# Optimization experiments

Measured on AMD Instinct MI355X. Metric: run time of the kernel, lower is better.

Reference implementation:

```python
import jax, jax.numpy as jnp
import numpy as np

B = 32768
N_TABLES = 26
N_ROWS = 200000
D = 64
N_DENSE = 13
NUM_PAIRS = (N_TABLES + 1) * N_TABLES // 2  # 351, pairs j < i over 27 vectors


def setup_inputs() -> dict:
    key = jax.random.key(0)
    ks = jax.random.split(key, 16)
    def lin(kw, kb, m, n):
        W = jax.random.normal(kw, (m, n), jnp.float32) * np.sqrt(2.0 / (m + n))
        b = jax.random.normal(kb, (m,), jnp.float32) * np.sqrt(1.0 / m)
        return W, b
    bw0, bb0 = lin(ks[0], ks[1], 512, N_DENSE)
    bw1, bb1 = lin(ks[2], ks[3], 256, 512)
    bw2, bb2 = lin(ks[4], ks[5], D, 256)
    tw0, tb0 = lin(ks[6], ks[7], 512, D + NUM_PAIRS)
    tw1, tb1 = lin(ks[8], ks[9], 256, 512)
    tw2, tb2 = lin(ks[10], ks[11], 1, 256)
    bound = np.sqrt(1.0 / N_ROWS)
    emb_tables = jax.random.uniform(ks[12], (N_TABLES, N_ROWS, D), jnp.float32,
                                    minval=-bound, maxval=bound)
    dense_x = jax.random.uniform(ks[13], (B, N_DENSE), jnp.float32)
    indices = jax.random.randint(ks[14], (N_TABLES, B), 0, N_ROWS, jnp.int64)
    return {"dense_x": dense_x, "indices": indices, "emb_tables": emb_tables,
            "bw0": bw0, "bb0": bb0, "bw1": bw1, "bb1": bb1, "bw2": bw2, "bb2": bb2,
            "tw0": tw0, "tb0": tb0, "tw1": tw1, "tb1": tb1, "tw2": tw2, "tb2": tb2}


def reference(dense_x, indices, emb_tables,
              bw0, bb0, bw1, bb1, bw2, bb2,
              tw0, tb0, tw1, tb1, tw2, tb2):
    # bottom MLP (all ReLU, sigmoid_bot = -1)
    h = jax.nn.relu(dense_x @ bw0.T + bb0)
    h = jax.nn.relu(h @ bw1.T + bb1)
    x_bot = jax.nn.relu(h @ bw2.T + bb2)          # [B, D]

    # multi-table EmbeddingBag(sum) with single-index bags -> plain gather
    embs = jax.vmap(lambda tbl, idx: tbl[idx])(emb_tables, indices)  # [26, B, D]

    # dot interaction over 27 feature vectors
    T = jnp.concatenate([x_bot[None], embs], axis=0).transpose(1, 0, 2)  # [B, 27, D]
    Z = jnp.einsum('bnd,bmd->bnm', T, T)                                 # [B, 27, 27]
    li, lj = jnp.tril_indices(N_TABLES + 1, k=-1)  # pairs with j < i (no self)
    Zflat = Z[:, li, lj]                           # [B, 351]
    R = jnp.concatenate([x_bot, Zflat], axis=1)    # [B, 415]

    # top MLP: ReLU, ReLU, Sigmoid (sigmoid_top = 2)
    h = jax.nn.relu(R @ tw0.T + tb0)
    h = jax.nn.relu(h @ tw1.T + tb1)
    p = jax.nn.sigmoid(h @ tw2.T + tb2)            # [B, 1]
    return p
```

## Files before the change

### kernel.cpp

```cpp
#include <hip/hip_runtime.h>
#include <cstddef>
#include <cstdint>

#define B_SZ    32768
#define NTAB    26
#define NROWS   200000

typedef __attribute__((ext_vector_type(8))) short short8v;
typedef __attribute__((ext_vector_type(4))) float f32x4;
typedef __attribute__((ext_vector_type(16))) float f32x16;

__device__ __forceinline__ ushort f2bf(float f) {
    uint32_t u = __builtin_bit_cast(uint32_t, f);
    u += 0x7FFFu + ((u >> 16) & 1u);
    return (ushort)(u >> 16);
}
__device__ __forceinline__ float bf2f(ushort h) {
    uint32_t u = ((uint32_t)h) << 16;
    return __builtin_bit_cast(float, u);
}
__device__ __forceinline__ void stage16(const ushort* g, ushort* l) {
    __builtin_amdgcn_global_load_lds(
        (const __attribute__((address_space(1))) unsigned int*)g,
        (__attribute__((address_space(3))) unsigned int*)l, 16, 0, 0);
}

__global__ __launch_bounds__(256) void conv_all_k(
    const float* __restrict__ dense_x, const float* __restrict__ bw0,
    const float* __restrict__ tw0, const float* __restrict__ bw1,
    const float* __restrict__ bw2, const float* __restrict__ tw1,
    ushort* __restrict__ dense_pad, ushort* __restrict__ bw0p,
    ushort* __restrict__ tw0p, ushort* __restrict__ bw1c,
    ushort* __restrict__ bw2c, ushort* __restrict__ tw1c)
{
    const int gid = blockIdx.x * 256 + threadIdx.x;
    if (gid < 1048576) {
        int r = gid >> 5, k = gid & 31;
        dense_pad[gid] = (k < 13) ? f2bf(dense_x[r * 13 + k]) : (ushort)0;
    } else if (gid < 1064960) {
        int i = gid - 1048576; int r = i >> 5, k = i & 31;
        bw0p[i] = (k < 13) ? f2bf(bw0[r * 13 + k]) : (ushort)0;
    } else if (gid < 1277952) {
        int i = gid - 1064960; int r = i / 416, k = i - r * 416;
        tw0p[i] = (k < 415) ? f2bf(tw0[r * 415 + k]) : (ushort)0;
    } else if (gid < 1409024) {
        int i = gid - 1277952; bw1c[i] = f2bf(bw1[i]);
    } else if (gid < 1425408) {
        int i = gid - 1409024; bw2c[i] = f2bf(bw2[i]);
    } else if (gid < 1556480) {
        int i = gid - 1425408; tw1c[i] = f2bf(tw1[i]);
    }
}

__global__ __launch_bounds__(256, 2) void bot012_k(
    const ushort* __restrict__ dense_pad, const ushort* __restrict__ bw0p,
    const float* __restrict__ bb0, const ushort* __restrict__ bw1c,
    const float* __restrict__ bb1, const ushort* __restrict__ bw2c,
    const float* __restrict__ bb2, ushort* __restrict__ Rb)
{
    __shared__ __align__(16) ushort h0s[32 * 512];
    __shared__ __align__(16) ushort Wst[256 * 32];
    __shared__ __align__(16) ushort h1s[32 * 256];
    const int t = threadIdx.x;
    const int lane = t & 63, w = t >> 6;
    const int fr = lane & 15, j16 = lane >> 4;
    const int bBase = blockIdx.x * 32;

    if (t < 128) {
        const int r = t >> 2, u = t & 3, us = u ^ ((r >> 1) & 3);
        stage16(dense_pad + (size_t)(bBase + r) * 32 + us * 8, &h1s[t * 8]);
    }

    f32x4 acc0[2][2][4] = {};
#pragma unroll
    for (int hh = 0; hh < 2; ++hh) {
#pragma unroll
        for (int i = 0; i < 4; ++i) {
            const int idx = i * 256 + t;
            const int r = idx >> 2, u = idx & 3, us = u ^ ((r >> 1) & 3);
            stage16(bw0p + (size_t)(hh * 256 + r) * 32 + us * 8, &Wst[idx * 8]);
        }
        __syncthreads();
        short8v a[2], b[4];
#pragma unroll
        for (int m = 0; m < 2; ++m) {
            const int r = m * 16 + fr;
            a[m] = *(const short8v*)&h1s[r * 32 + (j16 ^ ((r >> 1) & 3)) * 8];
        }
#pragma unroll
        for (int n = 0; n < 4; ++n) {
            const int lr = w * 64 + n * 16 + fr;
            b[n] = *(const short8v*)&Wst[lr * 32 + (j16 ^ ((lr >> 1) & 3)) * 8];
        }
        __builtin_amdgcn_s_setprio(1);
#pragma unroll
        for (int m = 0; m < 2; ++m)
#pragma unroll
            for (int n = 0; n < 4; ++n)
                acc0[hh][m][n] = __builtin_amdgcn_mfma_f32_16x16x32_bf16(b[n], a[m], acc0[hh][m][n], 0, 0, 0);
        __builtin_amdgcn_s_setprio(0);
        __syncthreads();
    }
#pragma unroll
    for (int hh = 0; hh < 2; ++hh)
#pragma unroll
    for (int n = 0; n < 4; ++n) {
        const int ch = hh * 256 + w * 64 + n * 16 + j16 * 4;
        const float4 bv = *(const float4*)&bb0[ch];
#pragma unroll
        for (int m = 0; m < 2; ++m) {
            const int s = m * 16 + fr;
            ushort4 o;
            o.x = f2bf(fmaxf(acc0[hh][m][n][0] + bv.x, 0.f));
            o.y = f2bf(fmaxf(acc0[hh][m][n][1] + bv.y, 0.f));
            o.z = f2bf(fmaxf(acc0[hh][m][n][2] + bv.z, 0.f));
            o.w = f2bf(fmaxf(acc0[hh][m][n][3] + bv.w, 0.f));
            const int u = ch >> 3, su = u ^ (s & 7);
            *(ushort4*)&h0s[s * 512 + su * 8 + (ch & 7)] = o;
        }
    }
    __syncthreads();

    f32x4 acc1[2][4] = {};
    for (int kt = 0; kt < 512; kt += 32) {
#pragma unroll
        for (int i = 0; i < 4; ++i) {
            const int idx = i * 256 + t;
            const int r = idx >> 2, u = idx & 3, us = u ^ ((r >> 1) & 3);
            stage16(bw1c + (size_t)r * 512 + kt + us * 8, &Wst[idx * 8]);
        }
        __syncthreads();
        short8v a[2], b[4];
#pragma unroll
        for (int m = 0; m < 2; ++m) {
            const int s = m * 16 + fr;
            const int u = (kt >> 3) + j16, su = u ^ (s & 7);
            a[m] = *(const short8v*)&h0s[s * 512 + su * 8];
        }
#pragma unroll
        for (int n = 0; n < 4; ++n) {
            const int lr = w * 64 + n * 16 + fr;
            b[n] = *(const short8v*)&Wst[lr * 32 + (j16 ^ ((lr >> 1) & 3)) * 8];
        }
        __builtin_amdgcn_s_setprio(1);
#pragma unroll
        for (int m = 0; m < 2; ++m)
#pragma unroll
            for (int n = 0; n < 4; ++n)
                acc1[m][n] = __builtin_amdgcn_mfma_f32_16x16x32_bf16(b[n], a[m], acc1[m][n], 0, 0, 0);
        __builtin_amdgcn_s_setprio(0);
        __syncthreads();
    }
#pragma unroll
    for (int n = 0; n < 4; ++n) {
        const int ch = w * 64 + n * 16 + j16 * 4;
        const float4 bv = *(const float4*)&bb1[ch];
#pragma unroll
        for (int m = 0; m < 2; ++m) {
            const int s = m * 16 + fr;
            ushort4 o;
            o.x = f2bf(fmaxf(acc1[m][n][0] + bv.x, 0.f));
            o.y = f2bf(fmaxf(acc1[m][n][1] + bv.y, 0.f));
            o.z = f2bf(fmaxf(acc1[m][n][2] + bv.z, 0.f));
            o.w = f2bf(fmaxf(acc1[m][n][3] + bv.w, 0.f));
            const int u = ch >> 3, su = u ^ (s & 7);
            *(ushort4*)&h1s[s * 256 + su * 8 + (ch & 7)] = o;
        }
    }
    __syncthreads();

    f32x4 acc2[2] = {};
    for (int kt = 0; kt < 256; kt += 32) {
        {
            const int r = t >> 2, u = t & 3, us = u ^ ((r >> 1) & 3);
            stage16(bw2c + (size_t)r * 256 + kt + us * 8, &Wst[t * 8]);
        }
        __syncthreads();
        short8v a[2], b;
#pragma unroll
        for (int m = 0; m < 2; ++m) {
            const int s = m * 16 + fr;
            const int u = (kt >> 3) + j16, su = u ^ (s & 7);
            a[m] = *(const short8v*)&h1s[s * 256 + su * 8];
        }
        {
            const int lr = w * 16 + fr;
            b = *(const short8v*)&Wst[lr * 32 + (j16 ^ ((lr >> 1) & 3)) * 8];
        }
#pragma unroll
        for (int m = 0; m < 2; ++m)
            acc2[m] = __builtin_amdgcn_mfma_f32_16x16x32_bf16(b, a[m], acc2[m], 0, 0, 0);
        __syncthreads();
    }
    {
        const int ch = w * 16 + j16 * 4;
        const float4 bv = *(const float4*)&bb2[ch];
#pragma unroll
        for (int m = 0; m < 2; ++m) {
            const int s = m * 16 + fr;
            ushort4 o;
            o.x = f2bf(fmaxf(acc2[m][0] + bv.x, 0.f));
            o.y = f2bf(fmaxf(acc2[m][1] + bv.y, 0.f));
            o.z = f2bf(fmaxf(acc2[m][2] + bv.z, 0.f));
            o.w = f2bf(fmaxf(acc2[m][3] + bv.w, 0.f));
            *(ushort4*)&Rb[(size_t)(bBase + s) * 64 + ch] = o;
        }
    }
}

__global__ __launch_bounds__(256, 3) void topint_k(
    const float* __restrict__ emb, const int* __restrict__ indices,
    const ushort* __restrict__ Rb, const ushort* __restrict__ tw0p,
    const float* __restrict__ tb0, const ushort* __restrict__ tw1c,
    const float* __restrict__ tb1, const float* __restrict__ tw2,
    const float* __restrict__ tb2, float* __restrict__ out)
{
    __shared__ __align__(16) ushort U[32 * 512];
    __shared__ __align__(16) ushort Wst[256 * 32];
    __shared__ __align__(16) int scratch[832];
    const int t = threadIdx.x;
    const int lane = t & 63, w = t >> 6;
    const int fr = lane & 15, j16 = lane >> 4;
    const int bBase = blockIdx.x * 32;

    {
        const int r = t >> 3, u = t & 7;
        short8v v = *(const short8v*)&Rb[(size_t)(bBase + r) * 64 + u * 8];
        *(short8v*)&U[r * 424 + u * 8] = v;
    }
    if (t < 32) U[t * 424 + 415] = 0;
    for (int e = t; e < 832; e += 256)
        scratch[e] = indices[(size_t)(e >> 5) * B_SZ + bBase + (e & 31)];
    __syncthreads();

    {
        const int r32 = lane & 31, half = lane >> 5;
        for (int it = 0; it < 8; ++it) {
            const int s = it * 4 + w;
            short8v tf[4];
            if (r32 == 0) {
#pragma unroll
                for (int kq = 0; kq < 4; ++kq)
                    tf[kq] = *(const short8v*)&U[s * 424 + kq * 16 + half * 8];
            } else if (r32 <= 26) {
                const int idxv = scratch[(r32 - 1) * 32 + s];
                const float* rp = emb + ((size_t)(r32 - 1) * NROWS + (size_t)idxv) * 64 + half * 8;
#pragma unroll
                for (int kq = 0; kq < 4; ++kq) {
                    const float4 x = *(const float4*)&rp[kq * 16];
                    const float4 y = *(const float4*)&rp[kq * 16 + 4];
                    short8v v;
                    v[0] = (short)f2bf(x.x); v[1] = (short)f2bf(x.y);
                    v[2] = (short)f2bf(x.z); v[3] = (short)f2bf(x.w);
                    v[4] = (short)f2bf(y.x); v[5] = (short)f2bf(y.y);
                    v[6] = (short)f2bf(y.z); v[7] = (short)f2bf(y.w);
                    tf[kq] = v;
                }
            } else {
#pragma unroll
                for (int kq = 0; kq < 4; ++kq) tf[kq] = (short8v)0;
            }
            f32x16 c = {};
#pragma unroll
            for (int kq = 0; kq < 4; ++kq)
                c = __builtin_amdgcn_mfma_f32_32x32x16_bf16(tf[kq], tf[kq], c, 0, 0, 0);
#pragma unroll
            for (int reg = 0; reg < 16; ++reg) {
                const int r = (reg & 3) + 8 * (reg >> 2) + 4 * half;
                if (r < 27 && r32 < r)
                    U[s * 424 + 64 + (r * (r - 1)) / 2 + r32] = f2bf(c[reg]);
            }
        }
    }
    __syncthreads();

    f32x4 accA[2][2][4] = {};
    for (int kt = 0; kt < 416; kt += 32) {
        short8v a[2];
#pragma unroll
        for (int m = 0; m < 2; ++m) {
            const int s = m * 16 + fr;
            a[m] = *(const short8v*)&U[s * 424 + ((kt >> 3) + j16) * 8];
        }
#pragma unroll
        for (int hh = 0; hh < 2; ++hh) {
#pragma unroll
            for (int i = 0; i < 4; ++i) {
                const int idx = i * 256 + t;
                const int r = idx >> 2, u = idx & 3, us = u ^ ((r >> 1) & 3);
                stage16(tw0p + (size_t)(hh * 256 + r) * 416 + kt + us * 8, &Wst[idx * 8]);
            }
            __syncthreads();
            short8v b[4];
#pragma unroll
            for (int n = 0; n < 4; ++n) {
                const int lr = w * 64 + n * 16 + fr;
                b[n] = *(const short8v*)&Wst[lr * 32 + (j16 ^ ((lr >> 1) & 3)) * 8];
            }
            __builtin_amdgcn_s_setprio(1);
#pragma unroll
            for (int m = 0; m < 2; ++m)
#pragma unroll
                for (int n = 0; n < 4; ++n)
                    accA[hh][m][n] = __builtin_amdgcn_mfma_f32_16x16x32_bf16(b[n], a[m], accA[hh][m][n], 0, 0, 0);
            __builtin_amdgcn_s_setprio(0);
            __syncthreads();
        }
    }
#pragma unroll
    for (int hh = 0; hh < 2; ++hh)
#pragma unroll
    for (int n = 0; n < 4; ++n) {
        const int ch = hh * 256 + w * 64 + n * 16 + j16 * 4;
        const float4 bv = *(const float4*)&tb0[ch];
#pragma unroll
        for (int m = 0; m < 2; ++m) {
            const int s = m * 16 + fr;
            ushort4 o;
            o.x = f2bf(fmaxf(accA[hh][m][n][0] + bv.x, 0.f));
            o.y = f2bf(fmaxf(accA[hh][m][n][1] + bv.y, 0.f));
            o.z = f2bf(fmaxf(accA[hh][m][n][2] + bv.z, 0.f));
            o.w = f2bf(fmaxf(accA[hh][m][n][3] + bv.w, 0.f));
            const int u = ch >> 3, su = u ^ (s & 7);
            *(ushort4*)&U[s * 512 + su * 8 + (ch & 7)] = o;
        }
    }
    __syncthreads();

    f32x4 acc2[2][4] = {};
    for (int kt = 0; kt < 512; kt += 32) {
#pragma unroll
        for (int i = 0; i < 4; ++i) {
            const int idx = i * 256 + t;
            const int r = idx >> 2, u = idx & 3, us = u ^ ((r >> 1) & 3);
            stage16(tw1c + (size_t)r * 512 + kt + us * 8, &Wst[idx * 8]);
        }
        __syncthreads();
        short8v a[2], b[4];
#pragma unroll
        for (int m = 0; m < 2; ++m) {
            const int s = m * 16 + fr;
            const int u = (kt >> 3) + j16, su = u ^ (s & 7);
            a[m] = *(const short8v*)&U[s * 512 + su * 8];
        }
#pragma unroll
        for (int n = 0; n < 4; ++n) {
            const int lr = w * 64 + n * 16 + fr;
            b[n] = *(const short8v*)&Wst[lr * 32 + (j16 ^ ((lr >> 1) & 3)) * 8];
        }
        __builtin_amdgcn_s_setprio(1);
#pragma unroll
        for (int m = 0; m < 2; ++m)
#pragma unroll
            for (int n = 0; n < 4; ++n)
                acc2[m][n] = __builtin_amdgcn_mfma_f32_16x16x32_bf16(b[n], a[m], acc2[m][n], 0, 0, 0);
        __builtin_amdgcn_s_setprio(0);
        __syncthreads();
    }

    float* red = (float*)scratch;
    float part[2] = {0.f, 0.f};
#pragma unroll
    for (int n = 0; n < 4; ++n) {
        const int ch = w * 64 + n * 16 + j16 * 4;
        const float4 bv = *(const float4*)&tb1[ch];
        const float4 wv = *(const float4*)&tw2[ch];
#pragma unroll
        for (int m = 0; m < 2; ++m) {
            part[m] += fmaxf(acc2[m][n][0] + bv.x, 0.f) * wv.x
                     + fmaxf(acc2[m][n][1] + bv.y, 0.f) * wv.y
                     + fmaxf(acc2[m][n][2] + bv.z, 0.f) * wv.z
                     + fmaxf(acc2[m][n][3] + bv.w, 0.f) * wv.w;
        }
    }
#pragma unroll
    for (int m = 0; m < 2; ++m) {
        float v = part[m];
        v += __shfl_xor(v, 16, 64);
        v += __shfl_xor(v, 32, 64);
        if (lane < 16) red[w * 32 + m * 16 + fr] = v;
    }
    __syncthreads();
    if (t < 32) {
        const float sm = red[t] + red[32 + t] + red[64 + t] + red[96 + t];
        out[bBase + t] = 1.f / (1.f + expf(-(sm + tb2[0])));
    }
}

extern "C" void kernel_launch(void* const* d_in, const int* in_sizes, int n_in,
                              void* d_out, int out_size, void* d_ws, size_t ws_size,
                              hipStream_t stream)
{
    (void)in_sizes; (void)n_in; (void)out_size; (void)ws_size;
    const float* dense_x = (const float*)d_in[0];
    const int*   indices = (const int*)d_in[1];
    const float* emb     = (const float*)d_in[2];
    const float* bw0 = (const float*)d_in[3];
    const float* bb0 = (const float*)d_in[4];
    const float* bw1 = (const float*)d_in[5];
    const float* bb1 = (const float*)d_in[6];
    const float* bw2 = (const float*)d_in[7];
    const float* bb2 = (const float*)d_in[8];
    const float* tw0 = (const float*)d_in[9];
    const float* tb0 = (const float*)d_in[10];
    const float* tw1 = (const float*)d_in[11];
    const float* tb1 = (const float*)d_in[12];
    const float* tw2 = (const float*)d_in[13];
    const float* tb2 = (const float*)d_in[14];
    float* out = (float*)d_out;

    ushort* ws16      = (ushort*)d_ws;
    ushort* dense_pad = ws16;
    ushort* Rb        = dense_pad + (size_t)B_SZ * 32;
    ushort* bw0p      = Rb + (size_t)B_SZ * 64;
    ushort* tw0p      = bw0p + 512 * 32;
    ushort* bw1c      = tw0p + 512 * 416;
    ushort* bw2c      = bw1c + 256 * 512;
    ushort* tw1c      = bw2c + 64 * 256;

    conv_all_k<<<dim3(6080), dim3(256), 0, stream>>>(
        dense_x, bw0, tw0, bw1, bw2, tw1,
        dense_pad, bw0p, tw0p, bw1c, bw2c, tw1c);

    bot012_k<<<dim3(B_SZ / 32), dim3(256), 0, stream>>>(
        dense_pad, bw0p, bb0, bw1c, bb1, bw2c, bb2, Rb);

    topint_k<<<dim3(B_SZ / 32), dim3(256), 0, stream>>>(
        emb, indices, Rb, tw0p, tb0, tw1c, tb1, tw2, tb2, out);
}
```

Baseline: 131.8 us.

## Double-buffer weight tiles in LDS to overlap staging with MFMA compute

Each weight-staging loop in both the bottom-MLP and top-MLP kernels now uses two LDS buffers. The next K-tile is prefetched via global_load_lds while the MFMAs run on the current tile, which drops one barrier per iteration and hides global load latency. The first tile of the next layer is also prefetched during the epilogue of the previous layer. The embedding gather now uses nontemporal loads, and topint_k's occupancy hint drops from 3 to 2 blocks/SM because the extra LDS buffer raises shared memory use.

```diff
diff --git a/kernel.cpp b/kernel.cpp
--- a/kernel.cpp
+++ b/kernel.cpp
@@ -59,7 +59,7 @@
     const float* __restrict__ bb2, ushort* __restrict__ Rb)
 {
     __shared__ __align__(16) ushort h0s[32 * 512];
-    __shared__ __align__(16) ushort Wst[256 * 32];
+    __shared__ __align__(16) ushort Wst[2][256 * 32];
     __shared__ __align__(16) ushort h1s[32 * 256];
     const int t = threadIdx.x;
     const int lane = t & 63, w = t >> 6;
@@ -70,17 +70,25 @@
         const int r = t >> 2, u = t & 3, us = u ^ ((r >> 1) & 3);
         stage16(dense_pad + (size_t)(bBase + r) * 32 + us * 8, &h1s[t * 8]);
     }
+#pragma unroll
+    for (int i = 0; i < 4; ++i) {
+        const int idx = i * 256 + t;
+        const int r = idx >> 2, u = idx & 3, us = u ^ ((r >> 1) & 3);
+        stage16(bw0p + (size_t)r * 32 + us * 8, &Wst[0][idx * 8]);
+    }
+    __syncthreads();
 
     f32x4 acc0[2][2][4] = {};
 #pragma unroll
     for (int hh = 0; hh < 2; ++hh) {
-#pragma unroll
-        for (int i = 0; i < 4; ++i) {
-            const int idx = i * 256 + t;
-            const int r = idx >> 2, u = idx & 3, us = u ^ ((r >> 1) & 3);
-            stage16(bw0p + (size_t)(hh * 256 + r) * 32 + us * 8, &Wst[idx * 8]);
-        }
-        __syncthreads();
+        if (hh == 0) {
+#pragma unroll
+            for (int i = 0; i < 4; ++i) {
+                const int idx = i * 256 + t;
+                const int r = idx >> 2, u = idx & 3, us = u ^ ((r >> 1) & 3);
+                stage16(bw0p + (size_t)(256 + r) * 32 + us * 8, &Wst[1][idx * 8]);
+            }
+        }
         short8v a[2], b[4];
 #pragma unroll
         for (int m = 0; m < 2; ++m) {
@@ -90,7 +98,7 @@
 #pragma unroll
         for (int n = 0; n < 4; ++n) {
             const int lr = w * 64 + n * 16 + fr;
-            b[n] = *(const short8v*)&Wst[lr * 32 + (j16 ^ ((lr >> 1) & 3)) * 8];
+            b[n] = *(const short8v*)&Wst[hh][lr * 32 + (j16 ^ ((lr >> 1) & 3)) * 8];
         }
         __builtin_amdgcn_s_setprio(1);
 #pragma unroll
@@ -99,7 +107,13 @@
             for (int n = 0; n < 4; ++n)
                 acc0[hh][m][n] = __builtin_amdgcn_mfma_f32_16x16x32_bf16(b[n], a[m], acc0[hh][m][n], 0, 0, 0);
         __builtin_amdgcn_s_setprio(0);
-        __syncthreads();
+        if (hh == 0) __syncthreads();
+    }
+#pragma unroll
+    for (int i = 0; i < 4; ++i) {
+        const int idx = i * 256 + t;
+        const int r = idx >> 2, u = idx & 3, us = u ^ ((r >> 1) & 3);
+        stage16(bw1c + (size_t)r * 512 + us * 8, &Wst[0][idx * 8]);
     }
 #pragma unroll
     for (int hh = 0; hh < 2; ++hh)
@@ -122,34 +136,45 @@
     __syncthreads();
 
     f32x4 acc1[2][4] = {};
-    for (int kt = 0; kt < 512; kt += 32) {
-#pragma unroll
-        for (int i = 0; i < 4; ++i) {
-            const int idx = i * 256 + t;
-            const int r = idx >> 2, u = idx & 3, us = u ^ ((r >> 1) & 3);
-            stage16(bw1c + (size_t)r * 512 + kt + us * 8, &Wst[idx * 8]);
-        }
-        __syncthreads();
-        short8v a[2], b[4];
-#pragma unroll
-        for (int m = 0; m < 2; ++m) {
-            const int s = m * 16 + fr;
-            const int u = (kt >> 3) + j16, su = u ^ (s & 7);
-            a[m] = *(const short8v*)&h0s[s * 512 + su * 8];
-        }
-#pragma unroll
-        for (int n = 0; n < 4; ++n) {
-            const int lr = w * 64 + n * 16 + fr;
-            b[n] = *(const short8v*)&Wst[lr * 32 + (j16 ^ ((lr >> 1) & 3)) * 8];
-        }
-        __builtin_amdgcn_s_setprio(1);
-#pragma unroll
-        for (int m = 0; m < 2; ++m)
-#pragma unroll
-            for (int n = 0; n < 4; ++n)
-                acc1[m][n] = __builtin_amdgcn_mfma_f32_16x16x32_bf16(b[n], a[m], acc1[m][n], 0, 0, 0);
-        __builtin_amdgcn_s_setprio(0);
-        __syncthreads();
+    {
+        int cur = 0;
+        for (int kt8 = 0; kt8 < 16; ++kt8) {
+            if (kt8 < 15) {
+                const int kt2 = (kt8 + 1) * 32;
+#pragma unroll
+                for (int i = 0; i < 4; ++i) {
+                    const int idx = i * 256 + t;
+                    const int r = idx >> 2, u = idx & 3, us = u ^ ((r >> 1) & 3);
+                    stage16(bw1c + (size_t)r * 512 + kt2 + us * 8, &Wst[cur ^ 1][idx * 8]);
+                }
+            }
+            const int kt = kt8 * 32;
+            short8v a[2], b[4];
+#pragma unroll
+            for (int m = 0; m < 2; ++m) {
+                const int s = m * 16 + fr;
+                const int u = (kt >> 3) + j16, su = u ^ (s & 7);
+                a[m] = *(const short8v*)&h0s[s * 512 + su * 8];
+            }
+#pragma unroll
+            for (int n = 0; n < 4; ++n) {
+                const int lr = w * 64 + n * 16 + fr;
+                b[n] = *(const short8v*)&Wst[cur][lr * 32 + (j16 ^ ((lr >> 1) & 3)) * 8];
+            }
+            __builtin_amdgcn_s_setprio(1);
+#pragma unroll
+            for (int m = 0; m < 2; ++m)
+#pragma unroll
+                for (int n = 0; n < 4; ++n)
+                    acc1[m][n] = __builtin_amdgcn_mfma_f32_16x16x32_bf16(b[n], a[m], acc1[m][n], 0, 0, 0);
+            __builtin_amdgcn_s_setprio(0);
+            __syncthreads();
+            cur ^= 1;
+        }
+    }
+    {
+        const int r = t >> 2, u = t & 3, us = u ^ ((r >> 1) & 3);
+        stage16(bw2c + (size_t)r * 256 + us * 8, &Wst[0][t * 8]);
     }
 #pragma unroll
     for (int n = 0; n < 4; ++n) {
@@ -170,27 +195,32 @@
     __syncthreads();
 
     f32x4 acc2[2] = {};
-    for (int kt = 0; kt < 256; kt += 32) {
-        {
-            const int r = t >> 2, u = t & 3, us = u ^ ((r >> 1) & 3);
-            stage16(bw2c + (size_t)r * 256 + kt + us * 8, &Wst[t * 8]);
-        }
-        __syncthreads();
-        short8v a[2], b;
-#pragma unroll
-        for (int m = 0; m < 2; ++m) {
-            const int s = m * 16 + fr;
-            const int u = (kt >> 3) + j16, su = u ^ (s & 7);
-            a[m] = *(const short8v*)&h1s[s * 256 + su * 8];
-        }
-        {
-            const int lr = w * 16 + fr;
-            b = *(const short8v*)&Wst[lr * 32 + (j16 ^ ((lr >> 1) & 3)) * 8];
-        }
-#pragma unroll
-        for (int m = 0; m < 2; ++m)
-            acc2[m] = __builtin_amdgcn_mfma_f32_16x16x32_bf16(b, a[m], acc2[m], 0, 0, 0);
-        __syncthreads();
+    {
+        int cur = 0;
+        for (int kt8 = 0; kt8 < 8; ++kt8) {
+            if (kt8 < 7) {
+                const int kt2 = (kt8 + 1) * 32;
+                const int r = t >> 2, u = t & 3, us = u ^ ((r >> 1) & 3);
+                stage16(bw2c + (size_t)r * 256 + kt2 + us * 8, &Wst[cur ^ 1][t * 8]);
+            }
+            const int kt = kt8 * 32;
+            short8v a[2], b;
+#pragma unroll
+            for (int m = 0; m < 2; ++m) {
+                const int s = m * 16 + fr;
+                const int u = (kt >> 3) + j16, su = u ^ (s & 7);
+                a[m] = *(const short8v*)&h1s[s * 256 + su * 8];
+            }
+            {
+                const int lr = w * 16 + fr;
+                b = *(const short8v*)&Wst[cur][lr * 32 + (j16 ^ ((lr >> 1) & 3)) * 8];
+            }
+#pragma unroll
+            for (int m = 0; m < 2; ++m)
+                acc2[m] = __builtin_amdgcn_mfma_f32_16x16x32_bf16(b, a[m], acc2[m], 0, 0, 0);
+            __syncthreads();
+            cur ^= 1;
+        }
     }
     {
         const int ch = w * 16 + j16 * 4;
@@ -208,7 +238,7 @@
     }
 }
 
-__global__ __launch_bounds__(256, 3) void topint_k(
+__global__ __launch_bounds__(256, 2) void topint_k(
     const float* __restrict__ emb, const int* __restrict__ indices,
     const ushort* __restrict__ Rb, const ushort* __restrict__ tw0p,
     const float* __restrict__ tb0, const ushort* __restrict__ tw1c,
@@ -216,7 +246,7 @@
     const float* __restrict__ tb2, float* __restrict__ out)
 {
     __shared__ __align__(16) ushort U[32 * 512];
-    __shared__ __align__(16) ushort Wst[256 * 32];
+    __shared__ __align__(16) ushort Wst[2][256 * 32];
     __shared__ __align__(16) int scratch[832];
     const int t = threadIdx.x;
     const int lane = t & 63, w = t >> 6;
@@ -233,6 +263,13 @@
         scratch[e] = indices[(size_t)(e >> 5) * B_SZ + bBase + (e & 31)];
     __syncthreads();
 
+#pragma unroll
+    for (int i = 0; i < 4; ++i) {
+        const int idx = i * 256 + t;
+        const int r = idx >> 2, u = idx & 3, us = u ^ ((r >> 1) & 3);
+        stage16(tw0p + (size_t)r * 416 + us * 8, &Wst[0][idx * 8]);
+    }
+
     {
         const int r32 = lane & 31, half = lane >> 5;
         for (int it = 0; it < 8; ++it) {
@@ -247,13 +284,13 @@
                 const float* rp = emb + ((size_t)(r32 - 1) * NROWS + (size_t)idxv) * 64 + half * 8;
 #pragma unroll
                 for (int kq = 0; kq < 4; ++kq) {
-                    const float4 x = *(const float4*)&rp[kq * 16];
-                    const float4 y = *(const float4*)&rp[kq * 16 + 4];
+                    const f32x4 x = __builtin_nontemporal_load((const f32x4*)&rp[kq * 16]);
+                    const f32x4 y = __builtin_nontemporal_load((const f32x4*)&rp[kq * 16 + 4]);
                     short8v v;
-                    v[0] = (short)f2bf(x.x); v[1] = (short)f2bf(x.y);
-                    v[2] = (short)f2bf(x.z); v[3] = (short)f2bf(x.w);
-                    v[4] = (short)f2bf(y.x); v[5] = (short)f2bf(y.y);
-                    v[6] = (short)f2bf(y.z); v[7] = (short)f2bf(y.w);
+                    v[0] = (short)f2bf(x[0]); v[1] = (short)f2bf(x[1]);
+                    v[2] = (short)f2bf(x[2]); v[3] = (short)f2bf(x[3]);
+                    v[4] = (short)f2bf(y[0]); v[5] = (short)f2bf(y[1]);
+                    v[6] = (short)f2bf(y[2]); v[7] = (short)f2bf(y[3]);
                     tf[kq] = v;
                 }
             } else {
@@ -275,27 +312,30 @@
     __syncthreads();
 
     f32x4 accA[2][2][4] = {};
-    for (int kt = 0; kt < 416; kt += 32) {
-        short8v a[2];
-#pragma unroll
-        for (int m = 0; m < 2; ++m) {
-            const int s = m * 16 + fr;
-            a[m] = *(const short8v*)&U[s * 424 + ((kt >> 3) + j16) * 8];
-        }
-#pragma unroll
-        for (int hh = 0; hh < 2; ++hh) {
-#pragma unroll
-            for (int i = 0; i < 4; ++i) {
-                const int idx = i * 256 + t;
-                const int r = idx >> 2, u = idx & 3, us = u ^ ((r >> 1) & 3);
-                stage16(tw0p + (size_t)(hh * 256 + r) * 416 + kt + us * 8, &Wst[idx * 8]);
-            }
-            __syncthreads();
-            short8v b[4];
+    {
+        int cur = 0;
+        for (int hi = 0; hi < 26; ++hi) {
+            const int kt = (hi >> 1) * 32, hh = hi & 1;
+            if (hi < 25) {
+                const int hi2 = hi + 1;
+                const int kt2 = (hi2 >> 1) * 32, hh2 = hi2 & 1;
+#pragma unroll
+                for (int i = 0; i < 4; ++i) {
+                    const int idx = i * 256 + t;
+                    const int r = idx >> 2, u = idx & 3, us = u ^ ((r >> 1) & 3);
+                    stage16(tw0p + (size_t)(hh2 * 256 + r) * 416 + kt2 + us * 8, &Wst[cur ^ 1][idx * 8]);
+                }
+            }
+            short8v a[2], b[4];
+#pragma unroll
+            for (int m = 0; m < 2; ++m) {
+                const int s = m * 16 + fr;
+                a[m] = *(const short8v*)&U[s * 424 + ((kt >> 3) + j16) * 8];
+            }
 #pragma unroll
             for (int n = 0; n < 4; ++n) {
                 const int lr = w * 64 + n * 16 + fr;
-                b[n] = *(const short8v*)&Wst[lr * 32 + (j16 ^ ((lr >> 1) & 3)) * 8];
+                b[n] = *(const short8v*)&Wst[cur][lr * 32 + (j16 ^ ((lr >> 1) & 3)) * 8];
             }
             __builtin_amdgcn_s_setprio(1);
 #pragma unroll
@@ -305,7 +345,14 @@
                     accA[hh][m][n] = __builtin_amdgcn_mfma_f32_16x16x32_bf16(b[n], a[m], accA[hh][m][n], 0, 0, 0);
             __builtin_amdgcn_s_setprio(0);
             __syncthreads();
-        }
+            cur ^= 1;
+        }
+    }
+#pragma unroll
+    for (int i = 0; i < 4; ++i) {
+        const int idx = i * 256 + t;
+        const int r = idx >> 2, u = idx & 3, us = u ^ ((r >> 1) & 3);
+        stage16(tw1c + (size_t)r * 512 + us * 8, &Wst[0][idx * 8]);
     }
 #pragma unroll
     for (int hh = 0; hh < 2; ++hh)
@@ -328,34 +375,41 @@
     __syncthreads();
 
     f32x4 acc2[2][4] = {};
-    for (int kt = 0; kt < 512; kt += 32) {
-#pragma unroll
-        for (int i = 0; i < 4; ++i) {
-            const int idx = i * 256 + t;
-            const int r = idx >> 2, u = idx & 3, us = u ^ ((r >> 1) & 3);
-            stage16(tw1c + (size_t)r * 512 + kt + us * 8, &Wst[idx * 8]);
-        }
-        __syncthreads();
-        short8v a[2], b[4];
-#pragma unroll
-        for (int m = 0; m < 2; ++m) {
-            const int s = m * 16 + fr;
-            const int u = (kt >> 3) + j16, su = u ^ (s & 7);
-            a[m] = *(const short8v*)&U[s * 512 + su * 8];
-        }
-#pragma unroll
-        for (int n = 0; n < 4; ++n) {
-            const int lr = w * 64 + n * 16 + fr;
-            b[n] = *(const short8v*)&Wst[lr * 32 + (j16 ^ ((lr >> 1) & 3)) * 8];
-        }
-        __builtin_amdgcn_s_setprio(1);
-#pragma unroll
-        for (int m = 0; m < 2; ++m)
-#pragma unroll
-            for (int n = 0; n < 4; ++n)
-                acc2[m][n] = __builtin_amdgcn_mfma_f32_16x16x32_bf16(b[n], a[m], acc2[m][n], 0, 0, 0);
-        __builtin_amdgcn_s_setprio(0);
-        __syncthreads();
+    {
+        int cur = 0;
+        for (int kt8 = 0; kt8 < 16; ++kt8) {
+            if (kt8 < 15) {
+                const int kt2 = (kt8 + 1) * 32;
+#pragma unroll
+                for (int i = 0; i < 4; ++i) {
+                    const int idx = i * 256 + t;
+                    const int r = idx >> 2, u = idx & 3, us = u ^ ((r >> 1) & 3);
+                    stage16(tw1c + (size_t)r * 512 + kt2 + us * 8, &Wst[cur ^ 1][idx * 8]);
+                }
+            }
+            const int kt = kt8 * 32;
+            short8v a[2], b[4];
+#pragma unroll
+            for (int m = 0; m < 2; ++m) {
+                const int s = m * 16 + fr;
+                const int u = (kt >> 3) + j16, su = u ^ (s & 7);
+                a[m] = *(const short8v*)&U[s * 512 + su * 8];
+            }
+#pragma unroll
+            for (int n = 0; n < 4; ++n) {
+                const int lr = w * 64 + n * 16 + fr;
+                b[n] = *(const short8v*)&Wst[cur][lr * 32 + (j16 ^ ((lr >> 1) & 3)) * 8];
+            }
+            __builtin_amdgcn_s_setprio(1);
+#pragma unroll
+            for (int m = 0; m < 2; ++m)
+#pragma unroll
+                for (int n = 0; n < 4; ++n)
+                    acc2[m][n] = __builtin_amdgcn_mfma_f32_16x16x32_bf16(b[n], a[m], acc2[m][n], 0, 0, 0);
+            __builtin_amdgcn_s_setprio(0);
+            __syncthreads();
+            cur ^= 1;
+        }
     }
 
     float* red = (float*)scratch;
```

New measurement: 155.3 us. 17.8% more time.
